# Kernel optimization log

Measured on AMD Instinct MI355X. Metric: run time of the kernel, lower is better.

The kernel has to match this reference:

```python
import jax, jax.numpy as jnp
import numpy as np

BIG = 2 ** 30  # sentinel label for background / padding


def _shift(a, dy, dx):
    # Shift last-two-dims image by (dy, dx), filling with BIG.
    H, W = a.shape[-2], a.shape[-1]
    pad = [(0, 0)] * (a.ndim - 2) + [(max(dy, 0), max(-dy, 0)), (max(dx, 0), max(-dx, 0))]
    ap = jnp.pad(a, pad, constant_values=BIG)
    ys, xs = max(-dy, 0), max(-dx, 0)
    return ap[..., ys:ys + H, xs:xs + W]


def _cc_counts(fg):
    # fg: bool [..., H, W]. Returns int32 [...] = number of 4-connected components
    # per image (== reduce_max of tfa.image.connected_components labels).
    H, W = fg.shape[-2], fg.shape[-1]
    idx = jnp.arange(H * W, dtype=jnp.int32).reshape(H, W)
    init = jnp.where(fg, idx, BIG)

    def step(lbl):
        nbr = jnp.minimum(jnp.minimum(_shift(lbl, 1, 0), _shift(lbl, -1, 0)),
                          jnp.minimum(_shift(lbl, 0, 1), _shift(lbl, 0, -1)))
        return jnp.where(fg, jnp.minimum(lbl, nbr), BIG)

    def cond(c):
        prev, cur = c
        return jnp.any(prev != cur)

    def body(c):
        _, cur = c
        return (cur, step(cur))

    _, final = jax.lax.while_loop(cond, body, (init, step(init)))
    # Each component's minimum-index pixel keeps its initial label -> one root per component.
    roots = fg & (final == init)
    return jnp.sum(roots.astype(jnp.int32), axis=(-2, -1))


def setup_inputs() -> dict:
    key = jax.random.key(0)
    # [n_color, n_box, batch, patches, H, W] binary images as float 0/1
    x = jax.random.randint(key, (2, 2, 8, 64, 64, 64), 0, 2).astype(jnp.float32)
    return {"x": x}


def reference(x) -> jnp.ndarray:
    fg = x > 0.5  # [C, B, batch, patches, H, W] boolean
    counts = _cc_counts(fg)  # [C, B, batch, patches] int32 component counts
    n_patches = counts.shape[-1]
    # tf.reduce_mean on int tensors truncates (integer division), then cast.
    mean_i = jnp.sum(counts, axis=-1) // n_patches  # [C, B, batch]
    return mean_i.astype(jnp.float32)
```

## Files before the change

### kernel.cpp

```cpp
#include <hip/hip_runtime.h>

constexpr int NPIX = 64 * 64;
constexpr int PATCHES = 64;
constexpr int RUNS_PER_ROW = 32;
constexpr int TABLE = 64 * RUNS_PER_ROW;

__device__ __forceinline__ int find_root(volatile int* p, int i) {
    while (true) {
        int pi = p[i];
        if (pi == i) return i;
        int gp = p[pi];
        if (gp == pi) return pi;
        p[i] = gp;
        i = gp;
    }
}

__device__ __forceinline__ int merge(int* p, int a, int b) {
    while (true) {
        a = find_root(p, a);
        b = find_root(p, b);
        if (a == b) return 0;
        if (a > b) { int t = a; a = b; b = t; }
        int old = atomicMin(&p[b], a);
        if (old == b) return 1;
        b = old;
    }
}

__global__ __launch_bounds__(256, 8) void cc_kernel(const float* __restrict__ in,
                                                    int* __restrict__ counts) {
    __shared__ int par[TABLE];
    __shared__ unsigned long long mrow[64];
    __shared__ int wpart[4];
    const int tid = threadIdx.x;
    const int img = blockIdx.x;

    const float4* base = reinterpret_cast<const float4*>(in + (size_t)img * NPIX);
    float4 v[4];
#pragma unroll
    for (int k = 0; k < 4; ++k) v[k] = base[k * 256 + tid];

    {
        int b0 = tid * 4;
        *reinterpret_cast<int4*>(&par[b0]) = make_int4(b0, b0 + 1, b0 + 2, b0 + 3);
        int b1 = 1024 + tid * 4;
        *reinterpret_cast<int4*>(&par[b1]) = make_int4(b1, b1 + 1, b1 + 2, b1 + 3);
    }

    const int w = tid >> 6;
    const int L = tid & 63;
    const int bg = L >> 4;
    const int j = L & 15;
#pragma unroll
    for (int k = 0; k < 4; ++k) {
        unsigned nib = (v[k].x > 0.5f ? 1u : 0u) | (v[k].y > 0.5f ? 2u : 0u) |
                       (v[k].z > 0.5f ? 4u : 0u) | (v[k].w > 0.5f ? 8u : 0u);
        unsigned long long c = (unsigned long long)nib << (4 * j);
#pragma unroll
        for (int d = 1; d < 16; d <<= 1) c |= __shfl_xor(c, d, 16);
        if (j == 0) mrow[16 * k + 4 * w + bg] = c;
    }
    __syncthreads();

    const int r = tid >> 2;
    const int q = tid & 3;
    const unsigned long long ma = mrow[r];
    const unsigned long long mb = (r < 63) ? mrow[r + 1] : 0ull;
    const unsigned long long sa = ma & ~(ma << 1);
    const unsigned long long sb = mb & ~(mb << 1);
    const unsigned long long qmask = 0xFFFFull << (16 * q);

    int cnt = __popcll(sa & qmask);

    unsigned long long both = ma & mb;
    unsigned long long ov = (both & ~(both << 1)) & qmask;
    while (ov) {
        int x = __builtin_ctzll(ov);
        ov &= ov - 1;
        unsigned long long below = (2ull << x) - 1;
        int ida = r * RUNS_PER_ROW + __popcll(sa & below) - 1;
        int idb = (r + 1) * RUNS_PER_ROW + __popcll(sb & below) - 1;
        cnt -= merge(par, ida, idb);
    }

#pragma unroll
    for (int d = 32; d > 0; d >>= 1) cnt += __shfl_xor(cnt, d, 64);
    if ((tid & 63) == 0) wpart[tid >> 6] = cnt;
    __syncthreads();
    if (tid == 0) counts[img] = wpart[0] + wpart[1] + wpart[2] + wpart[3];
}

__global__ void finalize_kernel(const int* __restrict__ counts,
                                float* __restrict__ out, int ngroups) {
    const int t = threadIdx.x;
    const int g = t >> 3, j = t & 7;
    if (g >= ngroups) return;
    const int* c = counts + g * PATCHES + j * 8;
    int s = 0;
#pragma unroll
    for (int k = 0; k < 8; ++k) s += c[k];
#pragma unroll
    for (int d = 4; d > 0; d >>= 1) s += __shfl_down(s, d, 8);
    if (j == 0) out[g] = (float)(s >> 6);
}

extern "C" void kernel_launch(void* const* d_in, const int* in_sizes, int n_in,
                              void* d_out, int out_size, void* d_ws, size_t ws_size,
                              hipStream_t stream) {
    const float* x = (const float*)d_in[0];
    float* out = (float*)d_out;
    int* counts = (int*)d_ws;

    const int nimg = in_sizes[0] / NPIX;
    const int ngroups = out_size;

    cc_kernel<<<nimg, 256, 0, stream>>>(x, counts);
    finalize_kernel<<<1, ngroups * 8, 0, stream>>>(counts, out, ngroups);
}
```

Baseline: 22.97 us.

## Merge row boundaries in hierarchical rounds to reduce union-find contention

Replaces the single pass, in which every thread merges its row with the next row all at once, with six rounds separated by barriers. Each round merges only the boundaries between pairs of blocks of rows whose size doubles each round, with one thread per boundary column. The goal is to keep union-find trees shallow and cut atomic contention and long find_root chains. It adds six __syncthreads and parallelizes per column bit instead of looping over overlaps, which raises idle-thread work in the later rounds.

```diff
diff --git a/kernel.cpp b/kernel.cpp
--- a/kernel.cpp
+++ b/kernel.cpp
@@ -2,8 +2,8 @@
 
 constexpr int NPIX = 64 * 64;
 constexpr int PATCHES = 64;
-constexpr int RUNS_PER_ROW = 32;
-constexpr int TABLE = 64 * RUNS_PER_ROW;
+constexpr int RPR = 32;
+constexpr int TABLE = 64 * RPR;
 
 __device__ __forceinline__ int find_root(volatile int* p, int i) {
     while (true) {
@@ -48,10 +48,7 @@
         *reinterpret_cast<int4*>(&par[b1]) = make_int4(b1, b1 + 1, b1 + 2, b1 + 3);
     }
 
-    const int w = tid >> 6;
-    const int L = tid & 63;
-    const int bg = L >> 4;
-    const int j = L & 15;
+    const int w = tid >> 6, L = tid & 63, bg = L >> 4, j = L & 15;
 #pragma unroll
     for (int k = 0; k < 4; ++k) {
         unsigned nib = (v[k].x > 0.5f ? 1u : 0u) | (v[k].y > 0.5f ? 2u : 0u) |
@@ -63,25 +60,33 @@
     }
     __syncthreads();
 
-    const int r = tid >> 2;
-    const int q = tid & 3;
-    const unsigned long long ma = mrow[r];
-    const unsigned long long mb = (r < 63) ? mrow[r + 1] : 0ull;
-    const unsigned long long sa = ma & ~(ma << 1);
-    const unsigned long long sb = mb & ~(mb << 1);
-    const unsigned long long qmask = 0xFFFFull << (16 * q);
+    int cnt;
+    {
+        const int r = tid >> 2, q = tid & 3;
+        const unsigned long long ma = mrow[r];
+        const unsigned long long sa = ma & ~(ma << 1);
+        cnt = __popcll(sa & (0xFFFFull << (16 * q)));
+    }
 
-    int cnt = __popcll(sa & qmask);
-
-    unsigned long long both = ma & mb;
-    unsigned long long ov = (both & ~(both << 1)) & qmask;
-    while (ov) {
-        int x = __builtin_ctzll(ov);
-        ov &= ov - 1;
-        unsigned long long below = (2ull << x) - 1;
-        int ida = r * RUNS_PER_ROW + __popcll(sa & below) - 1;
-        int idb = (r + 1) * RUNS_PER_ROW + __popcll(sb & below) - 1;
-        cnt -= merge(par, ida, idb);
+#pragma unroll
+    for (int k = 0; k < 6; ++k) {
+        const int cols = (32 >> k) << 6;
+        for (int c = tid; c < cols; c += 256) {
+            const int bi = c >> 6, bit = c & 63;
+            const int lo = bi * (2 << k) + (1 << k) - 1;
+            const unsigned long long ma = mrow[lo], mb = mrow[lo + 1];
+            const unsigned long long both = ma & mb;
+            const unsigned long long ov = both & ~(both << 1);
+            if ((ov >> bit) & 1ull) {
+                const unsigned long long below = (2ull << bit) - 1;
+                const unsigned long long sa = ma & ~(ma << 1);
+                const unsigned long long sb = mb & ~(mb << 1);
+                int ida = lo * RPR + __popcll(sa & below) - 1;
+                int idb = (lo + 1) * RPR + __popcll(sb & below) - 1;
+                cnt -= merge(par, ida, idb);
+            }
+        }
+        __syncthreads();
     }
 
 #pragma unroll
```

Result: slower. 35.23 us (+53.4%).
